# Kernel optimization log

Measured on AMD Instinct MI355X. Metric: run time of the kernel, lower is better.

The kernel has to match this reference:

```python
import jax, jax.numpy as jnp
import numpy as np

# constants from VMD_block.__init__ (K=4, alpha=2000, tau=0, DC=0, init=1, tol=5e-5, max_N=5)
K = 4
ALPHA = 2000.0
TAU = 0.0
TOL = 5e-05
MAX_N = 5


def _mvmd(f):
    """Multivariate VMD (Rehman & Aftab 2019) on f: (C, T) real signals.
    Returns modes u: (K, C, T). Shared center frequencies omega across channels."""
    C, T = f.shape
    half = T // 2
    T2 = 2 * T
    # mirror extension to length 2T
    fM = jnp.concatenate([f[:, :half][:, ::-1], f, f[:, half:][:, ::-1]], axis=1)
    freqs = (jnp.arange(1, T2 + 1, dtype=f.dtype) / T2) - 0.5 - (1.0 / T2)  # (T2,)
    f_hat = jnp.fft.fftshift(jnp.fft.fft(fM, axis=1), axes=1).astype(jnp.complex64)
    h2 = T2 // 2
    f_hat_plus = f_hat.at[:, :h2].set(0.0)  # keep analytic (positive-freq) part
    fpos = freqs[h2:]

    omega0 = (0.5 / K) * jnp.arange(K, dtype=f.dtype)  # init == 1, DC == 0
    u0 = jnp.zeros((K, C, T2), dtype=jnp.complex64)
    lam0 = jnp.zeros((C, T2), dtype=jnp.complex64)

    def cond(st):
        _, _, _, n, uDiff = st
        return jnp.logical_and(uDiff > TOL, n < MAX_N)

    def body(st):
        u, omega, lam, n, _ = st
        u_prev = u
        sum_all = jnp.sum(u, axis=0)  # (C, T2)
        for k in range(K):  # Gauss-Seidel mode updates; K is small & static
            sum_uk = sum_all - u[k]
            denom = 1.0 + ALPHA * (freqs - omega[k]) ** 2  # (T2,)
            u_k = (f_hat_plus - sum_uk - lam / 2.0) / denom
            sum_all = sum_uk + u_k
            u = u.at[k].set(u_k)
            power = jnp.abs(u_k[:, h2:]) ** 2  # (C, T2/2) positive freqs
            omega = omega.at[k].set(jnp.sum(fpos * power) / jnp.sum(power))
        lam = lam + TAU * (sum_all - f_hat_plus)  # tau == 0 -> dual ascent is a no-op
        d = u - u_prev
        uDiff = jnp.abs(jnp.sum(d * jnp.conj(d)) / T2) + jnp.finfo(jnp.float32).eps
        return u, omega, lam, n + 1, uDiff.astype(jnp.float32)

    st0 = (u0, omega0, lam0, jnp.int32(0), jnp.float32(TOL + 1.0))
    u, omega, lam, n, uDiff = jax.lax.while_loop(cond, body, st0)

    # rebuild full spectrum via Hermitian symmetry, back to time domain
    u_hat = jnp.zeros((K, C, T2), dtype=jnp.complex64)
    u_hat = u_hat.at[:, :, h2:].set(u[:, :, h2:])
    u_hat = u_hat.at[:, :, 1:h2 + 1].set(jnp.conj(u[:, :, h2:])[:, :, ::-1])
    u_hat = u_hat.at[:, :, 0].set(jnp.conj(u_hat[:, :, -1]))
    ut = jnp.real(jnp.fft.ifft(jnp.fft.ifftshift(u_hat, axes=-1), axis=-1))
    return ut[:, :, T2 // 4: 3 * T2 // 4]  # crop mirror padding -> (K, C, T)


def setup_inputs() -> dict:
    key = jax.random.key(0)
    x = jax.random.normal(key, (8, 2048, 64), dtype=jnp.float32)  # (B, T, C)
    return {"x": x}


def reference(x):
    B, T, C = x.shape
    xr = jnp.transpose(x, (0, 2, 1)).reshape(B * C, T)  # (B*C, T)
    u = _mvmd(xr)  # (K, B*C, T)
    x_l = jnp.transpose(u[0].reshape(B, C, T), (0, 2, 1))  # lowest-freq mode -> (B, T, C)
    x_h = x - x_l
    return (x_h, x_l)
```

## Files before the change

kernel.cpp:

```cpp
#include <hip/hip_runtime.h>
#include <math.h>

#define TLEN 2048
#define T2   4096
#define H2   2048
#define NBLK 512
#define EPS32 1.1920928955078125e-07

__device__ __forceinline__ double ld_acc(const double* p){
  return __hip_atomic_load(p, __ATOMIC_RELAXED, __HIP_MEMORY_SCOPE_AGENT);
}

__device__ __forceinline__ void gbar(unsigned* bar){
  __syncthreads();
  if (threadIdx.x == 0){
    __hip_atomic_fetch_add(bar, 1u, __ATOMIC_RELAXED, __HIP_MEMORY_SCOPE_AGENT);
    unsigned spins = 0;
    while (__hip_atomic_load(bar, __ATOMIC_RELAXED, __HIP_MEMORY_SCOPE_AGENT) < NBLK){
      if (++spins > (1u << 20)) break;
      __builtin_amdgcn_s_sleep(8);
    }
  }
  __syncthreads();
}

#define R2REG(ZA, ZB, W, SGN, E, O) {                           \
  float wy_ = (SGN) * W.y;                                      \
  E = make_float2(ZA.x + ZB.x, ZA.y + ZB.y);                    \
  float dx_ = ZA.x - ZB.x, dy_ = ZA.y - ZB.y;                   \
  O = make_float2(dx_ * W.x - dy_ * wy_, dx_ * wy_ + dy_ * W.x); }

#define R4REG(A, B, C, D, W1, W2, W3, SGN, Y0, Y1, Y2, Y3) {    \
  float w1y_ = (SGN)*W1.y, w2y_ = (SGN)*W2.y, w3y_ = (SGN)*W3.y;\
  float t0x = A.x + C.x, t0y = A.y + C.y;                       \
  float t1x = A.x - C.x, t1y = A.y - C.y;                       \
  float t2x = B.x + D.x, t2y = B.y + D.y;                       \
  float t3x = (SGN) * (B.y - D.y), t3y = -(SGN) * (B.x - D.x);  \
  Y0 = make_float2(t0x + t2x, t0y + t2y);                       \
  float y1x = t1x + t3x, y1y = t1y + t3y;                       \
  float y2x = t0x - t2x, y2y = t0y - t2y;                       \
  float y3x = t1x - t3x, y3y = t1y - t3y;                       \
  Y1 = make_float2(y1x*W1.x - y1y*w1y_, y1x*w1y_ + y1y*W1.x);   \
  Y2 = make_float2(y2x*W2.x - y2y*w2y_, y2x*w2y_ + y2y*W2.x);   \
  Y3 = make_float2(y3x*W3.x - y3y*w3y_, y3x*w3y_ + y3y*W3.x); }

__device__ __forceinline__ void fused2(float2 z0, float2 z1, float2 z2, float2 z3,
                                       float2 z4, float2 z5, float2 z6, float2 z7,
                                       const float2* twl, float sgn, float2* dst){
  const int tid = threadIdx.x;
  float2 wa = twl[2*tid], wb = twl[2*tid+512], wc = twl[2*tid+1024], wd = twl[2*tid+1536];
  float2 e0,o0,e1,o1,e2,o2,e3,o3;
  R2REG(z0, z4, wa, sgn, e0, o0)
  R2REG(z1, z5, wb, sgn, e1, o1)
  R2REG(z2, z6, wc, sgn, e2, o2)
  R2REG(z3, z7, wd, sgn, e3, o3)
  float2 w1 = twl[4*tid], w2 = twl[8*tid], w3 = twl[12*tid];
  float2 a0,a1,a2,a3, b0,b1,b2,b3;
  R4REG(e0, e1, e2, e3, w1, w2, w3, sgn, a0, a1, a2, a3)
  R4REG(o0, o1, o2, o3, w1, w2, w3, sgn, b0, b1, b2, b3)
  float4* d4 = reinterpret_cast<float4*>(dst + 8 * tid);
  d4[0] = make_float4(a0.x, a0.y, b0.x, b0.y);
  d4[1] = make_float4(a1.x, a1.y, b1.x, b1.y);
  d4[2] = make_float4(a2.x, a2.y, b2.x, b2.y);
  d4[3] = make_float4(a3.x, a3.y, b3.x, b3.y);
}

__device__ __forceinline__ void r4_stages(float2* src, float2* dst,
                                          const float2* twl, float sgn,
                                          int first, int cnt){
  const int tid = threadIdx.x;
  #pragma unroll 1
  for (int t = 0; t < cnt; ++t){
    const int L = 2 << (2 * (first + t));
    const int Lm = L - 1;
    #pragma unroll
    for (int bf = 0; bf < 2; ++bf){
      int idx = tid + (bf << 8);
      int q  = idx & Lm;
      int tb = idx - q;
      float2 a = src[idx];
      float2 b = src[idx + 512];
      float2 c = src[idx + 1024];
      float2 d = src[idx + 1536];
      float2 w1 = twl[2 * tb];
      float2 w2 = twl[4 * tb];
      float2 w3 = twl[6 * tb];
      float2 y0, y1, y2, y3;
      R4REG(a, b, c, d, w1, w2, w3, sgn, y0, y1, y2, y3)
      int ob = q + (tb << 2);
      dst[ob]         = y0;
      dst[ob + L]     = y1;
      dst[ob + 2 * L] = y2;
      dst[ob + 3 * L] = y3;
    }
    __syncthreads();
    float2* tt = src; src = dst; dst = tt;
  }
}

__device__ __forceinline__ double wred(double v){
  #pragma unroll
  for (int off = 32; off; off >>= 1) v += __shfl_down(v, off);
  return v;
}

__device__ __forceinline__ void red9(double a0, double a1, double a2, double a3,
                                     double a4, double a5, double a6, double a7,
                                     double a8, double* red, double* accs){
  const int tid = threadIdx.x, wave = tid >> 6, lane = tid & 63;
  double r;
  r = wred(a0); if (lane == 0) red[ 0 + wave] = r;
  r = wred(a1); if (lane == 0) red[ 4 + wave] = r;
  r = wred(a2); if (lane == 0) red[ 8 + wave] = r;
  r = wred(a3); if (lane == 0) red[12 + wave] = r;
  r = wred(a4); if (lane == 0) red[16 + wave] = r;
  r = wred(a5); if (lane == 0) red[20 + wave] = r;
  r = wred(a6); if (lane == 0) red[24 + wave] = r;
  r = wred(a7); if (lane == 0) red[28 + wave] = r;
  r = wred(a8); if (lane == 0) red[32 + wave] = r;
  __syncthreads();
  if (tid < 9)
    atomicAdd(&accs[tid], red[tid*4+0] + red[tid*4+1] + red[tid*4+2] + red[tid*4+3]);
}

#define MODE_S(UXc, UYc, OMc, AFP, AP) {                       \
  float ox_ = sx - (UXc), oy_ = sy - (UYc);                    \
  float d_  = fj - (OMc);                                      \
  float den_ = 1.0f + 2000.0f * d_ * d_;                       \
  float nx_ = (Fx - ox_) / den_, ny_ = (Fy - oy_) / den_;      \
  float pw_ = nx_ * nx_ + ny_ * ny_;                           \
  AFP += (double)(fj * pw_);  AP += (double)pw_;               \
  float ddx_ = nx_ - (UXc), ddy_ = ny_ - (UYc);                \
  aD += (double)(ddx_ * ddx_ + ddy_ * ddy_);                   \
  (UXc) = nx_; (UYc) = ny_;                                    \
  sx = ox_ + nx_; sy = oy_ + ny_; }

#define BIN_S(PP, FV, UX, UY) {                                \
  float Fx = FV.x, Fy = FV.y;                                  \
  float fj = (float)(tid + ((PP) << 8)) * (1.0f / 4096.0f);    \
  float sx = UX.x + UX.y + UX.z + UX.w;                        \
  float sy = UY.x + UY.y + UY.z + UY.w;                        \
  MODE_S(UX.x, UY.x, om.x, aFP0, aP0)                          \
  MODE_S(UX.y, UY.y, om.y, aFP1, aP1)                          \
  MODE_S(UX.z, UY.z, om.z, aFP2, aP2)                          \
  MODE_S(UX.w, UY.w, om.w, aFP3, aP3) }

#define IT1(PP, FV, UX, UY) { UX = make_float4(0.f,0.f,0.f,0.f); \
                              UY = make_float4(0.f,0.f,0.f,0.f); \
                              BIN_S(PP, FV, UX, UY) }

#define FCOMP(PP, FV) {                                        \
  int k = tid + ((PP) << 8);                                   \
  float2 A  = bufA[k];                                         \
  float2 Zm = bufA[(2048 - k) & 2047];                         \
  float px = 0.5f * (A.x + Zm.x), py = 0.5f * (A.y - Zm.y);    \
  float qx = 0.5f * (A.x - Zm.x), qy = 0.5f * (A.y + Zm.y);    \
  float2 W = twl[k];                                           \
  FV = make_float2(px + W.x * qy + W.y * qx,                   \
                   py - W.x * qx + W.y * qy); }

#define HERMU(PP, FV, UX, UY) {                                \
  int j = tid + ((PP) << 8);                                   \
  float vx, vy;                                                \
  if (act){                                                    \
    float sx = UX.y + UX.z + UX.w;                             \
    float sy = UY.y + UY.z + UY.w;                             \
    float fj = (float)j * (1.0f / 4096.0f);                    \
    float dd = fj - om0;                                       \
    float den = 1.0f + 2000.0f * dd * dd;                      \
    vx = (FV.x - sx) / den; vy = (FV.y - sy) / den;            \
  } else { vx = UX.x; vy = UY.x; }                             \
  bufA[j] = make_float2(vx, vy); }

#define ZPCOMP(PP, ZV) {                                       \
  int k = tid + ((PP) << 8);                                   \
  if (k == 0){                                                 \
    float e = bufA[0].x + bufA[2047].x;                        \
    float o = bufA[0].x - bufA[2047].x;                        \
    ZV = make_float2(e, o);                                    \
  } else {                                                     \
    float2 A  = bufA[k];                                       \
    float2 Bm = bufA[2048 - k];                                \
    float ex = A.x + Bm.x, ey = A.y - Bm.y;                    \
    float dx = A.x - Bm.x, dy = A.y + Bm.y;                    \
    float2 W = twl[k];                                         \
    float ox = dx * W.x + dy * W.y;                            \
    float oy = dy * W.x - dx * W.y;                            \
    ZV = make_float2(ex - oy, ey + ox);                        \
  } }

#define FOR8F(M) M(0,f0,ux0,uy0) M(1,f1,ux1,uy1) M(2,f2,ux2,uy2) M(3,f3,ux3,uy3) \
                 M(4,f4,ux4,uy4) M(5,f5,ux5,uy5) M(6,f6,ux6,uy6) M(7,f7,ux7,uy7)

#define ILAST(IDX, Y1, Y2) {                                   \
  float2 a = bufA[IDX];                                        \
  float2 bb = bufA[(IDX) + 512];                               \
  float2 c = bufA[(IDX) + 1024];                               \
  float2 d = bufA[(IDX) + 1536];                               \
  float t1x = a.x - c.x, t1y = a.y - c.y;                      \
  float t3x = -(bb.y - d.y), t3y = (bb.x - d.x);               \
  Y1 = make_float2(t1x + t3x, t1y + t3y);                      \
  float t0x = a.x + c.x, t0y = a.y + c.y;                      \
  float t2x = bb.x + d.x, t2y = bb.y + d.y;                    \
  Y2 = make_float2(t0x - t2x, t0y - t2y); }

__global__ void k_boot(float2* __restrict__ tw, unsigned* __restrict__ syncz){
  int p = blockIdx.x * 256 + threadIdx.x;
  double a = -6.283185307179586 * (double)p / 4096.0;
  tw[p] = make_float2((float)cos(a), (float)sin(a));
  if (blockIdx.x == 0 && threadIdx.x < 128) syncz[threadIdx.x] = 0u;
}

__global__ void __attribute__((amdgpu_flat_work_group_size(256, 256),
                               amdgpu_waves_per_eu(2, 2)))
k_main(const float* __restrict__ x, const float2* __restrict__ tw,
       unsigned* __restrict__ bar, double* __restrict__ accs,
       float* __restrict__ xh, float* __restrict__ xl){
  __shared__ float2 twl[3072];
  __shared__ float2 bufA[H2];
  __shared__ float2 bufB[H2];
  __shared__ double red[36];
  __shared__ float somf[8];
  const int tid = threadIdx.x;
  const int b = blockIdx.x & 7, ch = blockIdx.x >> 3;
  const float* xc = x + (size_t)b * TLEN * 64 + ch;

  #pragma unroll
  for (int i = 0; i < 12; ++i)
    twl[tid + (i << 8)] = tw[tid + (i << 8)];

  float2 z0, z1, z2, z3, z4, z5, z6, z7;
  z0 = make_float2(xc[(size_t)(1023 - 2*tid) * 64], xc[(size_t)(1022 - 2*tid) * 64]);
  z1 = make_float2(xc[(size_t)( 511 - 2*tid) * 64], xc[(size_t)( 510 - 2*tid) * 64]);
  { int t = 2*tid;        z2 = make_float2(xc[(size_t)t*64], xc[(size_t)(t+1)*64]); }
  { int t = 2*tid + 512;  z3 = make_float2(xc[(size_t)t*64], xc[(size_t)(t+1)*64]); }
  { int t = 2*tid + 1024; z4 = make_float2(xc[(size_t)t*64], xc[(size_t)(t+1)*64]); }
  { int t = 2*tid + 1536; z5 = make_float2(xc[(size_t)t*64], xc[(size_t)(t+1)*64]); }
  z6 = make_float2(xc[(size_t)(2047 - 2*tid) * 64], xc[(size_t)(2046 - 2*tid) * 64]);
  z7 = make_float2(xc[(size_t)(1535 - 2*tid) * 64], xc[(size_t)(1534 - 2*tid) * 64]);
  __syncthreads();

  fused2(z0, z1, z2, z3, z4, z5, z6, z7, twl, 1.0f, bufA);
  __syncthreads();
  r4_stages(bufA, bufB, twl, 1.0f, 1, 4);

  float2 f0, f1, f2, f3, f4, f5, f6, f7;
  FCOMP(0, f0) FCOMP(1, f1) FCOMP(2, f2) FCOMP(3, f3)
  FCOMP(4, f4) FCOMP(5, f5) FCOMP(6, f6) FCOMP(7, f7)

  float4 ux0, ux1, ux2, ux3, ux4, ux5, ux6, ux7;
  float4 uy0, uy1, uy2, uy3, uy4, uy5, uy6, uy7;
  float4 om = make_float4(0.0f, 0.125f, 0.25f, 0.375f);

  {
    double aFP0=0,aFP1=0,aFP2=0,aFP3=0,aP0=0,aP1=0,aP2=0,aP3=0,aD=0;
    FOR8F(IT1)
    red9(aFP0,aFP1,aFP2,aFP3,aP0,aP1,aP2,aP3,aD, red, accs);
  }

  bool active = true;
  double* slot = accs;
  #pragma unroll 1
  for (int it = 0; it < 3; ++it){
    gbar(bar + it);
    if (tid < 4) somf[tid] = (float)(ld_acc(slot + tid) / ld_acc(slot + 4 + tid));
    if (tid == 7) somf[7] = (ld_acc(slot + 8) * (1.0/4096.0) + EPS32 > 5e-5) ? 1.f : 0.f;
    __syncthreads();
    if (active){
      if (somf[7] != 0.0f){
        om.x = somf[0]; om.y = somf[1]; om.z = somf[2]; om.w = somf[3];
      } else active = false;
    }
    if (active){
      double aFP0=0,aFP1=0,aFP2=0,aFP3=0,aP0=0,aP1=0,aP2=0,aP3=0,aD=0;
      FOR8F(BIN_S)
      red9(aFP0,aFP1,aFP2,aFP3,aP0,aP1,aP2,aP3,aD, red, slot + 9);
    }
    slot += 9;
  }
  gbar(bar + 3);
  if (tid == 0) somf[0] = (float)(ld_acc(slot) / ld_acc(slot + 4));
  if (tid == 7) somf[7] = (ld_acc(slot + 8) * (1.0/4096.0) + EPS32 > 5e-5) ? 1.f : 0.f;
  __syncthreads();

  {
    bool act = active && (somf[7] != 0.0f);
    float om0 = somf[0];
    FOR8F(HERMU)
    __syncthreads();
    float2 p0, p1, p2, p3, p4, p5, p6, p7;
    ZPCOMP(0, p0) ZPCOMP(1, p1) ZPCOMP(2, p2) ZPCOMP(3, p3)
    ZPCOMP(4, p4) ZPCOMP(5, p5) ZPCOMP(6, p6) ZPCOMP(7, p7)
    __syncthreads();
    fused2(p0, p1, p2, p3, p4, p5, p6, p7, twl, -1.0f, bufB);
    __syncthreads();
    r4_stages(bufB, bufA, twl, -1.0f, 1, 3);
  }

  {
    const float scale = 1.0f / 4096.0f;
    float2 y1a, y2a, y1b, y2b;
    ILAST(tid,       y1a, y2a)
    ILAST(tid + 256, y1b, y2b)
    #define STOUT(YV, T0, ZS) {                                \
      size_t o0 = ((size_t)(b * TLEN + (T0))) * 64 + ch;       \
      float l0 = YV.x * scale, l1 = YV.y * scale;              \
      xh[o0]      = ZS.x - l0;  xl[o0]      = l0;              \
      xh[o0 + 64] = ZS.y - l1;  xl[o0 + 64] = l1; }
    STOUT(y1a, 2*tid,        z2)
    STOUT(y1b, 2*tid + 512,  z3)
    STOUT(y2a, 2*tid + 1024, z4)
    STOUT(y2b, 2*tid + 1536, z5)
  }
}

extern "C" void kernel_launch(void* const* d_in, const int* in_sizes, int n_in,
                              void* d_out, int out_size, void* d_ws, size_t ws_size,
                              hipStream_t stream){
  const float* x = (const float*)d_in[0];
  float* out_xh = (float*)d_out;
  float* out_xl = out_xh + (size_t)8 * TLEN * 64;

  char* ws = (char*)d_ws;
  float2* tw    = (float2*)ws;
  char*   sync  = ws + 32768;
  unsigned* bar = (unsigned*)sync;
  double* accs  = (double*)(sync + 128);

  k_boot<<<12, 256, 0, stream>>>(tw, (unsigned*)sync);
  k_main<<<NBLK, 256, 0, stream>>>(x, tw, bar, accs, out_xh, out_xl);
}
```

Before: 135.4 us.

## Use float per-thread accumulators, compute twiddles in-kernel, drop boot kernel

```diff
diff --git a/kernel.cpp b/kernel.cpp
--- a/kernel.cpp
+++ b/kernel.cpp
@@ -17,8 +17,8 @@
     __hip_atomic_fetch_add(bar, 1u, __ATOMIC_RELAXED, __HIP_MEMORY_SCOPE_AGENT);
     unsigned spins = 0;
     while (__hip_atomic_load(bar, __ATOMIC_RELAXED, __HIP_MEMORY_SCOPE_AGENT) < NBLK){
-      if (++spins > (1u << 20)) break;
-      __builtin_amdgcn_s_sleep(8);
+      if (++spins > (1u << 21)) break;
+      __builtin_amdgcn_s_sleep(2);
     }
   }
   __syncthreads();
@@ -98,29 +98,32 @@
   }
 }
 
-__device__ __forceinline__ double wred(double v){
+__device__ __forceinline__ float wredf(float v){
   #pragma unroll
   for (int off = 32; off; off >>= 1) v += __shfl_down(v, off);
   return v;
 }
 
-__device__ __forceinline__ void red9(double a0, double a1, double a2, double a3,
-                                     double a4, double a5, double a6, double a7,
-                                     double a8, double* red, double* accs){
+__device__ __forceinline__ void red9(float a0, float a1, float a2, float a3,
+                                     float a4, float a5, float a6, float a7,
+                                     float a8, float* redf, double* accs){
   const int tid = threadIdx.x, wave = tid >> 6, lane = tid & 63;
-  double r;
-  r = wred(a0); if (lane == 0) red[ 0 + wave] = r;
-  r = wred(a1); if (lane == 0) red[ 4 + wave] = r;
-  r = wred(a2); if (lane == 0) red[ 8 + wave] = r;
-  r = wred(a3); if (lane == 0) red[12 + wave] = r;
-  r = wred(a4); if (lane == 0) red[16 + wave] = r;
-  r = wred(a5); if (lane == 0) red[20 + wave] = r;
-  r = wred(a6); if (lane == 0) red[24 + wave] = r;
-  r = wred(a7); if (lane == 0) red[28 + wave] = r;
-  r = wred(a8); if (lane == 0) red[32 + wave] = r;
-  __syncthreads();
-  if (tid < 9)
-    atomicAdd(&accs[tid], red[tid*4+0] + red[tid*4+1] + red[tid*4+2] + red[tid*4+3]);
+  float r;
+  r = wredf(a0); if (lane == 0) redf[ 0 + wave] = r;
+  r = wredf(a1); if (lane == 0) redf[ 4 + wave] = r;
+  r = wredf(a2); if (lane == 0) redf[ 8 + wave] = r;
+  r = wredf(a3); if (lane == 0) redf[12 + wave] = r;
+  r = wredf(a4); if (lane == 0) redf[16 + wave] = r;
+  r = wredf(a5); if (lane == 0) redf[20 + wave] = r;
+  r = wredf(a6); if (lane == 0) redf[24 + wave] = r;
+  r = wredf(a7); if (lane == 0) redf[28 + wave] = r;
+  r = wredf(a8); if (lane == 0) redf[32 + wave] = r;
+  __syncthreads();
+  if (tid < 9){
+    double s = (double)redf[tid*4+0] + (double)redf[tid*4+1]
+             + (double)redf[tid*4+2] + (double)redf[tid*4+3];
+    atomicAdd(&accs[tid], s);
+  }
 }
 
 #define MODE_S(UXc, UYc, OMc, AFP, AP) {                       \
@@ -129,9 +132,9 @@
   float den_ = 1.0f + 2000.0f * d_ * d_;                       \
   float nx_ = (Fx - ox_) / den_, ny_ = (Fy - oy_) / den_;      \
   float pw_ = nx_ * nx_ + ny_ * ny_;                           \
-  AFP += (double)(fj * pw_);  AP += (double)pw_;               \
+  AFP += fj * pw_;  AP += pw_;                                 \
   float ddx_ = nx_ - (UXc), ddy_ = ny_ - (UYc);                \
-  aD += (double)(ddx_ * ddx_ + ddy_ * ddy_);                   \
+  aD += ddx_ * ddx_ + ddy_ * ddy_;                             \
   (UXc) = nx_; (UYc) = ny_;                                    \
   sx = ox_ + nx_; sy = oy_ + ny_; }
 
@@ -204,30 +207,27 @@
   float t2x = bb.x + d.x, t2y = bb.y + d.y;                    \
   Y2 = make_float2(t0x - t2x, t0y - t2y); }
 
-__global__ void k_boot(float2* __restrict__ tw, unsigned* __restrict__ syncz){
-  int p = blockIdx.x * 256 + threadIdx.x;
-  double a = -6.283185307179586 * (double)p / 4096.0;
-  tw[p] = make_float2((float)cos(a), (float)sin(a));
-  if (blockIdx.x == 0 && threadIdx.x < 128) syncz[threadIdx.x] = 0u;
-}
-
 __global__ void __attribute__((amdgpu_flat_work_group_size(256, 256),
                                amdgpu_waves_per_eu(2, 2)))
-k_main(const float* __restrict__ x, const float2* __restrict__ tw,
-       unsigned* __restrict__ bar, double* __restrict__ accs,
-       float* __restrict__ xh, float* __restrict__ xl){
+k_main(const float* __restrict__ x, unsigned* __restrict__ bar,
+       double* __restrict__ accs, float* __restrict__ xh, float* __restrict__ xl){
   __shared__ float2 twl[3072];
   __shared__ float2 bufA[H2];
   __shared__ float2 bufB[H2];
-  __shared__ double red[36];
+  __shared__ float redf[36];
   __shared__ float somf[8];
   const int tid = threadIdx.x;
   const int b = blockIdx.x & 7, ch = blockIdx.x >> 3;
   const float* xc = x + (size_t)b * TLEN * 64 + ch;
 
   #pragma unroll
-  for (int i = 0; i < 12; ++i)
-    twl[tid + (i << 8)] = tw[tid + (i << 8)];
+  for (int i = 0; i < 12; ++i){
+    int p = tid + (i << 8);
+    float ang = (float)(-1.5339807878856412e-3 * (double)p);
+    float s, c;
+    sincosf(ang, &s, &c);
+    twl[p] = make_float2(c, s);
+  }
 
   float2 z0, z1, z2, z3, z4, z5, z6, z7;
   z0 = make_float2(xc[(size_t)(1023 - 2*tid) * 64], xc[(size_t)(1022 - 2*tid) * 64]);
@@ -253,9 +253,9 @@
   float4 om = make_float4(0.0f, 0.125f, 0.25f, 0.375f);
 
   {
-    double aFP0=0,aFP1=0,aFP2=0,aFP3=0,aP0=0,aP1=0,aP2=0,aP3=0,aD=0;
+    float aFP0=0,aFP1=0,aFP2=0,aFP3=0,aP0=0,aP1=0,aP2=0,aP3=0,aD=0;
     FOR8F(IT1)
-    red9(aFP0,aFP1,aFP2,aFP3,aP0,aP1,aP2,aP3,aD, red, accs);
+    red9(aFP0,aFP1,aFP2,aFP3,aP0,aP1,aP2,aP3,aD, redf, accs);
   }
 
   bool active = true;
@@ -272,9 +272,9 @@
       } else active = false;
     }
     if (active){
-      double aFP0=0,aFP1=0,aFP2=0,aFP3=0,aP0=0,aP1=0,aP2=0,aP3=0,aD=0;
+      float aFP0=0,aFP1=0,aFP2=0,aFP3=0,aP0=0,aP1=0,aP2=0,aP3=0,aD=0;
       FOR8F(BIN_S)
-      red9(aFP0,aFP1,aFP2,aFP3,aP0,aP1,aP2,aP3,aD, red, slot + 9);
+      red9(aFP0,aFP1,aFP2,aFP3,aP0,aP1,aP2,aP3,aD, redf, slot + 9);
     }
     slot += 9;
   }
@@ -322,11 +322,9 @@
   float* out_xl = out_xh + (size_t)8 * TLEN * 64;
 
   char* ws = (char*)d_ws;
-  float2* tw    = (float2*)ws;
-  char*   sync  = ws + 32768;
-  unsigned* bar = (unsigned*)sync;
-  double* accs  = (double*)(sync + 128);
-
-  k_boot<<<12, 256, 0, stream>>>(tw, (unsigned*)sync);
-  k_main<<<NBLK, 256, 0, stream>>>(x, tw, bar, accs, out_xh, out_xl);
-}
+  unsigned* bar = (unsigned*)ws;
+  double* accs  = (double*)(ws + 128);
+
+  hipMemsetAsync(ws, 0, 512, stream);
+  k_main<<<NBLK, 256, 0, stream>>>(x, bar, accs, out_xh, out_xl);
+}
```

New measurement: 133.0 us. Within noise of the previous version (-1.8%).
